# Kernel optimization log

Measured on AMD Instinct MI355X. Metric: run time of the kernel, lower is better.

Reference implementation:

```python
import jax, jax.numpy as jnp
import numpy as np

N_OBS = 6000
N_X = 6000
D_FEAT = 16
N_DOM = 3


def _block_ranges(n, d):
    b = np.linspace(0, n, d + 1).astype(np.int32)
    return jnp.asarray(np.stack([b[:-1], b[1:]], axis=1))  # [d,2] (start,end)


def setup_inputs() -> dict:
    key = jax.random.key(0)
    ks = jax.random.split(key, 6)
    xobs = jax.random.normal(ks[0], (N_OBS, D_FEAT), jnp.float32)
    x = jax.random.normal(ks[1], (N_X, D_FEAT), jnp.float32)
    w = jnp.round(jax.random.uniform(ks[2], (N_X, 1), jnp.float32))  # binary treatment
    alpha0 = jax.random.uniform(ks[3], (N_OBS, 1), jnp.float32)
    alpha1 = jax.random.uniform(ks[4], (N_OBS, 1), jnp.float32)
    n_pairs = N_DOM * (N_DOM - 1) // 2
    transfer_factor_logit = 0.1 * jax.random.normal(ks[5], (n_pairs,), jnp.float32)
    raw_lengthscale = jnp.zeros((), jnp.float32)  # gpytorch raw param; softplus(0)~0.693
    return {
        "xobs": xobs, "x": x, "w": w,
        "alpha0": alpha0, "alpha1": alpha1,
        "transfer_factor_logit": transfer_factor_logit,
        "raw_lengthscale": raw_lengthscale,
        "domain_ranges_obs": _block_ranges(N_OBS, N_DOM),
        "domain_ranges_x": _block_ranges(N_X, N_DOM),
    }


def _matern52(x1, x2, lengthscale):
    # gpytorch MaternKernel(nu=5/2): k(d)=(1+sqrt5*d+5/3*d^2)exp(-sqrt5*d), d=||x1-x2||/ls
    x1 = x1 / lengthscale
    x2 = x2 / lengthscale
    sq = (jnp.sum(x1 * x1, 1)[:, None] + jnp.sum(x2 * x2, 1)[None, :]
          - 2.0 * (x1 @ x2.T))
    d = jnp.sqrt(jnp.maximum(sq, 1e-12))
    s5d = jnp.sqrt(jnp.asarray(5.0, d.dtype)) * d
    return (1.0 + s5d + (5.0 / 3.0) * d * d) * jnp.exp(-s5d)


def _domain_ids(n, ranges):
    # contiguous sorted partition: id = #starts <= idx  - 1
    idx = jnp.arange(n)
    return jnp.sum(idx[:, None] >= ranges[None, :, 0], axis=1) - 1


def reference(xobs, x, w, alpha0, alpha1, transfer_factor_logit,
              raw_lengthscale, domain_ranges_obs, domain_ranges_x):
    ls = jax.nn.softplus(raw_lengthscale)
    M = _matern52(xobs, x, ls)                       # [N_obs, N_x]
    # pairwise transfer factor matrix F[di,dj]: 1 on diagonal, sigmoid(logit_n)
    # for pair n enumerated as (i<j) row-major, matching the original loop order
    tf = jax.nn.sigmoid(transfer_factor_logit)
    iu, ju = np.triu_indices(N_DOM, 1)
    F = jnp.ones((N_DOM, N_DOM), M.dtype).at[iu, ju].set(tf).at[ju, iu].set(tf)
    dom_o = _domain_ids(xobs.shape[0], domain_ranges_obs)   # [N_obs]
    dom_x = _domain_ids(x.shape[0], domain_ranges_x)        # [N_x]
    K = M * F[dom_o[:, None], dom_x[None, :]]               # fused transfer blend
    f0 = alpha0[:, 0] @ K                                   # [N_x]
    f1 = alpha1[:, 0] @ K
    wv = w.reshape(-1)
    return wv * f0 + (1.0 - wv) * f1
```

## Files before the change

### kernel.cpp

```cpp
#include <hip/hip_runtime.h>
#include <math.h>

typedef _Float16 f16x8 __attribute__((ext_vector_type(8)));
typedef float    f32x4 __attribute__((ext_vector_type(4)));

__global__ __launch_bounds__(256) void prep_all(
    const float* __restrict__ xobs, const float* __restrict__ x,
    const float* __restrict__ alpha0, const float* __restrict__ alpha1,
    const float* __restrict__ tfl, const float* __restrict__ rawls,
    const int* __restrict__ rngo,
    _Float16* __restrict__ ap, _Float16* __restrict__ bh, _Float16* __restrict__ bl,
    float* __restrict__ no5, float* __restrict__ nx5,
    float* __restrict__ a0f, float* __restrict__ a1f,
    int n_obs, int n_x)
{
    const int t   = threadIdx.x;
    const int r   = t >> 4;
    const int k   = t & 15;
    const int row = blockIdx.x * 16 + r;

    const float rv = rawls[0];
    const float ls = fmaxf(rv, 0.f) + log1pf(__expf(-fabsf(rv)));
    const float s5_ls2 = 5.f / (ls * ls);

    if (row < n_obs) {
        const float v = xobs[(size_t)row * 16 + k];
        float nv = v * v;
        nv += __shfl_xor(nv, 1, 64);
        nv += __shfl_xor(nv, 2, 64);
        nv += __shfl_xor(nv, 4, 64);
        nv += __shfl_xor(nv, 8, 64);
        const _Float16 h = (_Float16)v;
        ap[(size_t)row * 32 + k]      = h;
        ap[(size_t)row * 32 + 16 + k] = (_Float16)(v - (float)h);
        if (k == 0) no5[row] = nv * s5_ls2;
        if (k == 1) {
            const float t0 = 1.f / (1.f + __expf(-tfl[0]));
            const float t1 = 1.f / (1.f + __expf(-tfl[1]));
            const float t2 = 1.f / (1.f + __expf(-tfl[2]));
            const int dom = (row >= rngo[2] ? 1 : 0) + (row >= rngo[4] ? 1 : 0);
            const float F0 = (dom == 0) ? 1.f : ((dom == 1) ? t0 : t1);
            const float F1 = (dom == 0) ? t0  : ((dom == 1) ? 1.f : t2);
            const float F2 = (dom == 0) ? t1  : ((dom == 1) ? t2  : 1.f);
            const float av0 = alpha0[row], av1 = alpha1[row];
            a0f[row]             = av0 * F0;
            a0f[n_obs + row]     = av0 * F1;
            a0f[2 * n_obs + row] = av0 * F2;
            a1f[row]             = av1 * F0;
            a1f[n_obs + row]     = av1 * F1;
            a1f[2 * n_obs + row] = av1 * F2;
        }
    }
    if (row < n_x) {
        const float v = x[(size_t)row * 16 + k];
        float nv = v * v;
        nv += __shfl_xor(nv, 1, 64);
        nv += __shfl_xor(nv, 2, 64);
        nv += __shfl_xor(nv, 4, 64);
        nv += __shfl_xor(nv, 8, 64);
        const _Float16 h = (_Float16)v;
        bh[(size_t)row * 16 + k] = h;
        bl[(size_t)row * 16 + k] = (_Float16)(v - (float)h);
        if (k == 0) nx5[row] = nv * s5_ls2;
    }
}

__global__ __launch_bounds__(256, 8) void matern_mfma(
    const _Float16* __restrict__ ap, const _Float16* __restrict__ bh,
    const _Float16* __restrict__ bl,
    const float* __restrict__ no5, const float* __restrict__ nx5,
    const float* __restrict__ a0f, const float* __restrict__ a1f,
    const float* __restrict__ rawls, const int* __restrict__ rngx,
    float* __restrict__ f01, int n_obs, int n_x, int ntiles_i, int tiles_per_chunk)
{
    const int wave = threadIdx.x >> 6;
    const int lane = threadIdx.x & 63;
    const int njt  = n_x >> 4;
    const int jt   = blockIdx.x * 4 + wave;
    if (jt >= njt) return;
    const int g16 = lane >> 4;
    const int l16 = lane & 15;
    const int j   = jt * 16 + l16;

    const f16x8 B1 = *(const f16x8*)(bh + (size_t)j * 16 + (g16 & 1) * 8);
    f16x8 B2 = f16x8{0, 0, 0, 0, 0, 0, 0, 0};
    if (g16 < 2) B2 = *(const f16x8*)(bl + (size_t)j * 16 + g16 * 8);

    const float rv = rawls[0];
    const float ls = fmaxf(rv, 0.f) + log1pf(__expf(-fabsf(rv)));
    const float c2_5 = -10.f / (ls * ls);
    const float nx5j = nx5[j];

    const int dxj = (j >= rngx[2] ? 1 : 0) + (j >= rngx[4] ? 1 : 0);
    const float* __restrict__ a0p = a0f + (size_t)dxj * n_obs;
    const float* __restrict__ a1p = a1f + (size_t)dxj * n_obs;

    const float C13  = 1.f / 3.f;
    const float NL2E = -1.4426950408889634f;

    float s0 = 0.f, s1 = 0.f;
    const int it0 = blockIdx.y * tiles_per_chunk;
    const int it1 = min(it0 + tiles_per_chunk, ntiles_i);

    for (int it = it0; it < it1; ++it) {
        const int ia = it * 16;
        const f16x8 Aa = *(const f16x8*)(ap + (size_t)(ia + l16) * 32 + g16 * 8);
        const int ra = ia + g16 * 4;
        const f32x4 nov = *(const f32x4*)(no5 + ra);
        const f32x4 a0v = *(const f32x4*)(a0p + ra);
        const f32x4 a1v = *(const f32x4*)(a1p + ra);

        f32x4 acc = {0.f, 0.f, 0.f, 0.f};
        acc = __builtin_amdgcn_mfma_f32_16x16x32_f16(Aa, B1, acc, 0, 0, 0);
        acc = __builtin_amdgcn_mfma_f32_16x16x32_f16(Aa, B2, acc, 0, 0, 0);

        #pragma unroll
        for (int rr = 0; rr < 4; ++rr) {
            float u = fmaf(c2_5, acc[rr], nov[rr] + nx5j);
            u = fmaxf(u, 1e-11f);
            const float rs   = __frsqrt_rn(u);
            const float s5d  = u * rs;
            const float poly = fmaf(C13, u, 1.f + s5d);
            const float e    = __builtin_amdgcn_exp2f(NL2E * s5d);
            const float m    = poly * e;
            s0 = fmaf(a0v[rr], m, s0);
            s1 = fmaf(a1v[rr], m, s1);
        }
    }

    s0 += __shfl_xor(s0, 16, 64);
    s0 += __shfl_xor(s0, 32, 64);
    s1 += __shfl_xor(s1, 16, 64);
    s1 += __shfl_xor(s1, 32, 64);
    if (g16 == 0) {
        atomicAdd(&f01[j], s0);
        atomicAdd(&f01[n_x + j], s1);
    }
}

__global__ void combine_out(const float* __restrict__ w,
                            const float* __restrict__ f01,
                            float* __restrict__ out, int n_x)
{
    const int j = blockIdx.x * 256 + threadIdx.x;
    if (j < n_x) {
        const float wv = w[j];
        out[j] = wv * f01[j] + (1.f - wv) * f01[n_x + j];
    }
}

extern "C" void kernel_launch(void* const* d_in, const int* in_sizes, int n_in,
                              void* d_out, int out_size, void* d_ws, size_t ws_size,
                              hipStream_t stream)
{
    const float* xobs = (const float*)d_in[0];
    const float* x    = (const float*)d_in[1];
    const float* w    = (const float*)d_in[2];
    const float* a0   = (const float*)d_in[3];
    const float* a1   = (const float*)d_in[4];
    const float* tfl  = (const float*)d_in[5];
    const float* rls  = (const float*)d_in[6];
    const int*   rngo = (const int*)d_in[7];
    const int*   rngx = (const int*)d_in[8];

    const int n_obs = in_sizes[0] / 16;
    const int n_x   = in_sizes[1] / 16;

    char* p = (char*)d_ws;
    auto take = [&](size_t bytes) { char* q = p; p += (bytes + 255) & ~(size_t)255; return q; };
    float*     f01 = (float*)    take(sizeof(float) * 2 * (size_t)n_x);
    _Float16*  ap  = (_Float16*) take(sizeof(_Float16) * 32 * (size_t)n_obs);
    _Float16*  bh  = (_Float16*) take(sizeof(_Float16) * 16 * (size_t)n_x);
    _Float16*  bl  = (_Float16*) take(sizeof(_Float16) * 16 * (size_t)n_x);
    float*     no5 = (float*)    take(sizeof(float) * (size_t)n_obs);
    float*     nx5 = (float*)    take(sizeof(float) * (size_t)n_x);
    float*     a0f = (float*)    take(sizeof(float) * 3 * (size_t)n_obs);
    float*     a1f = (float*)    take(sizeof(float) * 3 * (size_t)n_obs);

    (void)hipMemsetAsync(f01, 0, sizeof(float) * 2 * (size_t)n_x, stream);

    const int nmax = (n_obs > n_x) ? n_obs : n_x;
    prep_all<<<(nmax + 15) / 16, 256, 0, stream>>>(
        xobs, x, a0, a1, tfl, rls, rngo, ap, bh, bl, no5, nx5, a0f, a1f, n_obs, n_x);

    const int njt = n_x / 16;
    const int ntiles_i = n_obs / 16;
    const int tiles_per_chunk = 15;
    const int gy = (ntiles_i + tiles_per_chunk - 1) / tiles_per_chunk;
    dim3 grid((njt + 3) / 4, gy);
    matern_mfma<<<grid, 256, 0, stream>>>(ap, bh, bl, no5, nx5, a0f, a1f, rls,
                                          rngx, f01, n_obs, n_x,
                                          ntiles_i, tiles_per_chunk);

    combine_out<<<(n_x + 255) / 256, 256, 0, stream>>>(w, f01, (float*)d_out, n_x);
}
```

Before: 99.93 us.

## Register-block four column tiles per wave and compute transfer factors inline

Each wave now processes four 16-column tiles, so every loaded A fragment, obs norm and alpha vector is reused across four pairs of MFMAs instead of one. The per-domain alpha*F precompute in the prep kernel is removed. The transfer factor is now picked per tile in the main loop from sigmoid values computed once per wave, which assumes domain boundaries align to 16-row tiles. The row chunk drops from 15 to 8 tiles and the occupancy hint drops to 4, trading register pressure and more atomics per output for better operand reuse.

```diff
diff --git a/kernel.cpp b/kernel.cpp
--- a/kernel.cpp
+++ b/kernel.cpp
@@ -6,12 +6,9 @@
 
 __global__ __launch_bounds__(256) void prep_all(
     const float* __restrict__ xobs, const float* __restrict__ x,
-    const float* __restrict__ alpha0, const float* __restrict__ alpha1,
-    const float* __restrict__ tfl, const float* __restrict__ rawls,
-    const int* __restrict__ rngo,
+    const float* __restrict__ rawls,
     _Float16* __restrict__ ap, _Float16* __restrict__ bh, _Float16* __restrict__ bl,
     float* __restrict__ no5, float* __restrict__ nx5,
-    float* __restrict__ a0f, float* __restrict__ a1f,
     int n_obs, int n_x)
 {
     const int t   = threadIdx.x;
@@ -34,22 +31,6 @@
         ap[(size_t)row * 32 + k]      = h;
         ap[(size_t)row * 32 + 16 + k] = (_Float16)(v - (float)h);
         if (k == 0) no5[row] = nv * s5_ls2;
-        if (k == 1) {
-            const float t0 = 1.f / (1.f + __expf(-tfl[0]));
-            const float t1 = 1.f / (1.f + __expf(-tfl[1]));
-            const float t2 = 1.f / (1.f + __expf(-tfl[2]));
-            const int dom = (row >= rngo[2] ? 1 : 0) + (row >= rngo[4] ? 1 : 0);
-            const float F0 = (dom == 0) ? 1.f : ((dom == 1) ? t0 : t1);
-            const float F1 = (dom == 0) ? t0  : ((dom == 1) ? 1.f : t2);
-            const float F2 = (dom == 0) ? t1  : ((dom == 1) ? t2  : 1.f);
-            const float av0 = alpha0[row], av1 = alpha1[row];
-            a0f[row]             = av0 * F0;
-            a0f[n_obs + row]     = av0 * F1;
-            a0f[2 * n_obs + row] = av0 * F2;
-            a1f[row]             = av1 * F0;
-            a1f[n_obs + row]     = av1 * F1;
-            a1f[2 * n_obs + row] = av1 * F2;
-        }
     }
     if (row < n_x) {
         const float v = x[(size_t)row * 16 + k];
@@ -65,40 +46,60 @@
     }
 }
 
-__global__ __launch_bounds__(256, 8) void matern_mfma(
+__global__ __launch_bounds__(256, 4) void matern_mfma(
     const _Float16* __restrict__ ap, const _Float16* __restrict__ bh,
     const _Float16* __restrict__ bl,
     const float* __restrict__ no5, const float* __restrict__ nx5,
-    const float* __restrict__ a0f, const float* __restrict__ a1f,
-    const float* __restrict__ rawls, const int* __restrict__ rngx,
+    const float* __restrict__ alpha0, const float* __restrict__ alpha1,
+    const float* __restrict__ tfl, const float* __restrict__ rawls,
+    const int* __restrict__ rngo, const int* __restrict__ rngx,
     float* __restrict__ f01, int n_obs, int n_x, int ntiles_i, int tiles_per_chunk)
 {
     const int wave = threadIdx.x >> 6;
     const int lane = threadIdx.x & 63;
     const int njt  = n_x >> 4;
-    const int jt   = blockIdx.x * 4 + wave;
-    if (jt >= njt) return;
+    const int jt0  = (blockIdx.x * 4 + wave) * 4;
+    if (jt0 >= njt) return;
     const int g16 = lane >> 4;
     const int l16 = lane & 15;
-    const int j   = jt * 16 + l16;
-
-    const f16x8 B1 = *(const f16x8*)(bh + (size_t)j * 16 + (g16 & 1) * 8);
-    f16x8 B2 = f16x8{0, 0, 0, 0, 0, 0, 0, 0};
-    if (g16 < 2) B2 = *(const f16x8*)(bl + (size_t)j * 16 + g16 * 8);
 
     const float rv = rawls[0];
     const float ls = fmaxf(rv, 0.f) + log1pf(__expf(-fabsf(rv)));
     const float c2_5 = -10.f / (ls * ls);
-    const float nx5j = nx5[j];
-
-    const int dxj = (j >= rngx[2] ? 1 : 0) + (j >= rngx[4] ? 1 : 0);
-    const float* __restrict__ a0p = a0f + (size_t)dxj * n_obs;
-    const float* __restrict__ a1p = a1f + (size_t)dxj * n_obs;
+
+    const float t0 = 1.f / (1.f + __expf(-tfl[0]));
+    const float t1 = 1.f / (1.f + __expf(-tfl[1]));
+    const float t2 = 1.f / (1.f + __expf(-tfl[2]));
+    const int ro2 = rngo[2], ro4 = rngo[4];
+    const int rx2 = rngx[2], rx4 = rngx[4];
+
+    f16x8 B1[4], B2[4];
+    float nxj[4];
+    float Fc0[4], Fc1[4], Fc2[4];
+    int   jv[4];
+    #pragma unroll
+    for (int t = 0; t < 4; ++t) {
+        const int jt  = jt0 + t;
+        const bool ok = (jt < njt);
+        const int jc  = ok ? jt * 16 + l16 : l16;
+        jv[t] = ok ? jc : -1;
+        B1[t] = *(const f16x8*)(bh + (size_t)jc * 16 + (g16 & 1) * 8);
+        B2[t] = f16x8{0, 0, 0, 0, 0, 0, 0, 0};
+        if (g16 < 2) B2[t] = *(const f16x8*)(bl + (size_t)jc * 16 + g16 * 8);
+        nxj[t] = nx5[jc];
+        const int jb  = jt * 16;
+        const int dxj = (jb >= rx2 ? 1 : 0) + (jb >= rx4 ? 1 : 0);
+        Fc0[t] = (dxj == 0) ? 1.f : ((dxj == 1) ? t0 : t1);
+        Fc1[t] = (dxj == 0) ? t0  : ((dxj == 1) ? 1.f : t2);
+        Fc2[t] = (dxj == 0) ? t1  : ((dxj == 1) ? t2  : 1.f);
+    }
 
     const float C13  = 1.f / 3.f;
     const float NL2E = -1.4426950408889634f;
 
-    float s0 = 0.f, s1 = 0.f;
+    float s0[4] = {0.f, 0.f, 0.f, 0.f};
+    float s1[4] = {0.f, 0.f, 0.f, 0.f};
+
     const int it0 = blockIdx.y * tiles_per_chunk;
     const int it1 = min(it0 + tiles_per_chunk, ntiles_i);
 
@@ -107,34 +108,52 @@
         const f16x8 Aa = *(const f16x8*)(ap + (size_t)(ia + l16) * 32 + g16 * 8);
         const int ra = ia + g16 * 4;
         const f32x4 nov = *(const f32x4*)(no5 + ra);
-        const f32x4 a0v = *(const f32x4*)(a0p + ra);
-        const f32x4 a1v = *(const f32x4*)(a1p + ra);
-
-        f32x4 acc = {0.f, 0.f, 0.f, 0.f};
-        acc = __builtin_amdgcn_mfma_f32_16x16x32_f16(Aa, B1, acc, 0, 0, 0);
-        acc = __builtin_amdgcn_mfma_f32_16x16x32_f16(Aa, B2, acc, 0, 0, 0);
+        const f32x4 a0v = *(const f32x4*)(alpha0 + ra);
+        const f32x4 a1v = *(const f32x4*)(alpha1 + ra);
+
+        const int dmi = (ia >= ro2 ? 1 : 0) + (ia >= ro4 ? 1 : 0);
+        float fd[4];
+        #pragma unroll
+        for (int t = 0; t < 4; ++t)
+            fd[t] = (dmi == 0) ? Fc0[t] : ((dmi == 1) ? Fc1[t] : Fc2[t]);
+
+        f32x4 acc[4];
+        #pragma unroll
+        for (int t = 0; t < 4; ++t) {
+            f32x4 a = {0.f, 0.f, 0.f, 0.f};
+            a = __builtin_amdgcn_mfma_f32_16x16x32_f16(Aa, B1[t], a, 0, 0, 0);
+            a = __builtin_amdgcn_mfma_f32_16x16x32_f16(Aa, B2[t], a, 0, 0, 0);
+            acc[t] = a;
+        }
 
         #pragma unroll
         for (int rr = 0; rr < 4; ++rr) {
-            float u = fmaf(c2_5, acc[rr], nov[rr] + nx5j);
-            u = fmaxf(u, 1e-11f);
-            const float rs   = __frsqrt_rn(u);
-            const float s5d  = u * rs;
-            const float poly = fmaf(C13, u, 1.f + s5d);
-            const float e    = __builtin_amdgcn_exp2f(NL2E * s5d);
-            const float m    = poly * e;
-            s0 = fmaf(a0v[rr], m, s0);
-            s1 = fmaf(a1v[rr], m, s1);
+            #pragma unroll
+            for (int t = 0; t < 4; ++t) {
+                float u = fmaf(c2_5, acc[t][rr], nov[rr] + nxj[t]);
+                u = fmaxf(u, 1e-11f);
+                const float rs   = __frsqrt_rn(u);
+                const float s5d  = u * rs;
+                const float poly = fmaf(C13, u, 1.f + s5d);
+                const float e    = __builtin_amdgcn_exp2f(NL2E * s5d);
+                const float m    = poly * e;
+                s0[t] = fmaf(fd[t] * a0v[rr], m, s0[t]);
+                s1[t] = fmaf(fd[t] * a1v[rr], m, s1[t]);
+            }
         }
     }
 
-    s0 += __shfl_xor(s0, 16, 64);
-    s0 += __shfl_xor(s0, 32, 64);
-    s1 += __shfl_xor(s1, 16, 64);
-    s1 += __shfl_xor(s1, 32, 64);
-    if (g16 == 0) {
-        atomicAdd(&f01[j], s0);
-        atomicAdd(&f01[n_x + j], s1);
+    #pragma unroll
+    for (int t = 0; t < 4; ++t) {
+        float a = s0[t], b = s1[t];
+        a += __shfl_xor(a, 16, 64);
+        a += __shfl_xor(a, 32, 64);
+        b += __shfl_xor(b, 16, 64);
+        b += __shfl_xor(b, 32, 64);
+        if (g16 == 0 && jv[t] >= 0) {
+            atomicAdd(&f01[jv[t]], a);
+            atomicAdd(&f01[n_x + jv[t]], b);
+        }
     }
 }
 
@@ -174,22 +193,21 @@
     _Float16*  bl  = (_Float16*) take(sizeof(_Float16) * 16 * (size_t)n_x);
     float*     no5 = (float*)    take(sizeof(float) * (size_t)n_obs);
     float*     nx5 = (float*)    take(sizeof(float) * (size_t)n_x);
-    float*     a0f = (float*)    take(sizeof(float) * 3 * (size_t)n_obs);
-    float*     a1f = (float*)    take(sizeof(float) * 3 * (size_t)n_obs);
 
     (void)hipMemsetAsync(f01, 0, sizeof(float) * 2 * (size_t)n_x, stream);
 
     const int nmax = (n_obs > n_x) ? n_obs : n_x;
     prep_all<<<(nmax + 15) / 16, 256, 0, stream>>>(
-        xobs, x, a0, a1, tfl, rls, rngo, ap, bh, bl, no5, nx5, a0f, a1f, n_obs, n_x);
-
-    const int njt = n_x / 16;
+        xobs, x, rls, ap, bh, bl, no5, nx5, n_obs, n_x);
+
+    const int njt      = n_x / 16;
     const int ntiles_i = n_obs / 16;
-    const int tiles_per_chunk = 15;
+    const int tiles_per_chunk = 8;
     const int gy = (ntiles_i + tiles_per_chunk - 1) / tiles_per_chunk;
-    dim3 grid((njt + 3) / 4, gy);
-    matern_mfma<<<grid, 256, 0, stream>>>(ap, bh, bl, no5, nx5, a0f, a1f, rls,
-                                          rngx, f01, n_obs, n_x,
+    const int gx = (njt + 15) / 16;
+    dim3 grid(gx, gy);
+    matern_mfma<<<grid, 256, 0, stream>>>(ap, bh, bl, no5, nx5, a0, a1, tfl, rls,
+                                          rngo, rngx, f01, n_obs, n_x,
                                           ntiles_i, tiles_per_chunk);
 
     combine_out<<<(n_x + 255) / 256, 256, 0, stream>>>(w, f01, (float*)d_out, n_x);
```

Measured after the change: 100.7 us. Within noise of the previous version (+0.8%).
